# Optimization experiments

Measured on AMD Instinct MI355X. Metric: run time of the kernel, lower is better.

The kernel has to match this reference:

```python
import jax, jax.numpy as jnp
import numpy as np

B, F_IN, T_IN = 256, 3, 800
C, K, H, N_OUT = 128, 15, 150, 10

def hard_sigmoid(x):
    # Keras-style hard sigmoid used by LSTMHardSigmoid: clamp(0.2*x + 0.5, 0, 1)
    return jnp.clip(0.2 * x + 0.5, 0.0, 1.0)

def setup_inputs() -> dict:
    key = jax.random.key(0)
    ks = jax.random.split(key, 16)
    mk = lambda k, s, sc=0.05: (jax.random.normal(k, s, dtype=jnp.float32) * sc)
    return {
        "x": jax.random.normal(ks[0], (B, F_IN, T_IN), dtype=jnp.float32),
        "conv_w": mk(ks[1], (C, F_IN, K), 0.1),
        "conv_b": jnp.zeros((C,), jnp.float32),
        # PyTorch LSTM layout: [4H, in] with gate order i,f,g,o
        "w_ih_f": mk(ks[2], (4 * H, C)),
        "w_hh_f": mk(ks[3], (4 * H, H)),
        "b_ih_f": mk(ks[4], (4 * H,)),
        "b_hh_f": mk(ks[5], (4 * H,)),
        "w_ih_b": mk(ks[6], (4 * H, C)),
        "w_hh_b": mk(ks[7], (4 * H, H)),
        "b_ih_b": mk(ks[8], (4 * H,)),
        "b_hh_b": mk(ks[9], (4 * H,)),
        "lin1_w": mk(ks[10], (50, 2 * H)),
        "lin1_b": jnp.zeros((50,), jnp.float32),
        "lin2_w": mk(ks[11], (N_OUT, 50)),
        "lin2_b": jnp.zeros((N_OUT,), jnp.float32),
    }

def _lstm_dir(xseq, w_ih, w_hh, b_ih, b_hh, reverse):
    # xseq: [B, T, C] -> pre-activations [B, T, 4H]
    pre = jnp.einsum('btc,gc->btg', xseq, w_ih) + b_ih + b_hh
    pre_t = jnp.swapaxes(pre, 0, 1)  # [T, B, 4H]
    h0 = jnp.zeros((xseq.shape[0], H), pre.dtype)
    c0 = jnp.zeros((xseq.shape[0], H), pre.dtype)
    def step(carry, gt):
        h, c = carry
        g = gt + h @ w_hh.T
        i, f, gg, o = jnp.split(g, 4, axis=-1)
        c = hard_sigmoid(f) * c + hard_sigmoid(i) * jnp.tanh(gg)
        h = hard_sigmoid(o) * jnp.tanh(c)
        return (h, c), h
    _, hs = jax.lax.scan(step, (h0, c0), pre_t, reverse=reverse)
    return jnp.swapaxes(hs, 0, 1)  # [B, T, H]

def reference(x, conv_w, conv_b, w_ih_f, w_hh_f, b_ih_f, b_hh_f,
              w_ih_b, w_hh_b, b_ih_b, b_hh_b, lin1_w, lin1_b, lin2_w, lin2_b):
    # net1: Conv1d (VALID) + ReLU + (Dropout: identity at eval) + MaxPool1d(2)
    y = jax.lax.conv_general_dilated(
        x, conv_w, window_strides=(1,), padding='VALID',
        dimension_numbers=('NCH', 'OIH', 'NCH')) + conv_b[None, :, None]
    y = jax.nn.relu(y)                       # [B, 128, 786]
    L = y.shape[2] // 2
    y = y[:, :, :2 * L].reshape(y.shape[0], y.shape[1], L, 2).max(axis=-1)  # [B,128,393]
    xseq = jnp.transpose(y, (0, 2, 1))       # [B, 393, 128]
    # net2: bidirectional LSTM with hard-sigmoid gates
    h_fwd = _lstm_dir(xseq, w_ih_f, w_hh_f, b_ih_f, b_hh_f, reverse=False)
    h_bwd = _lstm_dir(xseq, w_ih_b, w_hh_b, b_ih_b, b_hh_b, reverse=True)
    bi = jnp.concatenate([h_fwd, h_bwd], axis=-1)  # [B, T, 300]
    # global max-pool over time (F.max_pool1d with kernel = full length)
    pooled = bi.max(axis=1)                  # [B, 300]
    # net3: Linear + ReLU + (Dropout identity) + Linear + Softmax(dim=1)
    z = jax.nn.relu(pooled @ lin1_w.T + lin1_b)
    logits = z @ lin2_w.T + lin2_b
    return jax.nn.softmax(logits, axis=1)
```

## Files before the change

kernel.cpp:

```cpp
#include <hip/hip_runtime.h>
#include <cstdio>

#define BATCH 256
#define TSEQ  393
#define CH    128
#define FIN   3
#define TIN   800
#define KK    15
#define HID   150
#define NPAD  640
#define KPAD  160
#define NB    16
#define PHASE 131
#define SLOTSTRIDE (256*640)

typedef _Float16 half_t;
typedef __attribute__((ext_vector_type(8))) _Float16 h8v;
typedef __attribute__((ext_vector_type(4))) _Float16 h4v;
typedef __attribute__((ext_vector_type(4))) float f4v;

__device__ inline float hsig(float x){
  return __builtin_amdgcn_fmed3f(fmaf(0.2f, x, 0.5f), 0.f, 1.f);
}
__device__ inline float tanh_(float x){
  float e = __expf(2.f*x);
  return fmaf(-2.f, __builtin_amdgcn_rcpf(e + 1.f), 1.f);
}

__global__ __launch_bounds__(256) void setup(const float* __restrict__ x,
    const float* __restrict__ conv_w, const float* __restrict__ conv_b,
    const float* __restrict__ wihf, const float* __restrict__ whhf,
    const float* __restrict__ bihf, const float* __restrict__ bhhf,
    const float* __restrict__ wihb, const float* __restrict__ whhb,
    const float* __restrict__ bihb, const float* __restrict__ bhhb,
    half_t* __restrict__ xseq, half_t* __restrict__ wih, half_t* __restrict__ whh,
    float* __restrict__ bsum){
  __shared__ float wl[CH*FIN*KK];
  __shared__ float xl[FIN][78];
  int bx = blockIdx.x, tid = threadIdx.x;
  if (bx < 3328){
    int b = bx & 255, t0 = (bx >> 8)*32;
    for (int i = tid; i < CH*FIN*KK; i += 256) wl[i] = conv_w[i];
    int p0 = 2*t0;
    for (int i = tid; i < FIN*78; i += 256){
      int f = i/78, q = i%78; int p = p0 + q;
      xl[f][q] = (p < TIN) ? x[((size_t)b*FIN + f)*TIN + p] : 0.f;
    }
    __syncthreads();
    int c = tid & 127, th = tid >> 7;
    float a0[16], a1[16];
    #pragma unroll
    for (int i=0;i<16;++i){ a0[i]=0.f; a1[i]=0.f; }
    #pragma unroll
    for (int f=0; f<FIN; ++f){
      float xv[46];
      #pragma unroll
      for (int q=0;q<46;++q) xv[q] = xl[f][th*32 + q];
      #pragma unroll
      for (int k=0;k<KK;++k){
        float ws = wl[c*FIN*KK + f*KK + k];
        #pragma unroll
        for (int i=0;i<16;++i){
          a0[i] = fmaf(xv[2*i+k],   ws, a0[i]);
          a1[i] = fmaf(xv[2*i+k+1], ws, a1[i]);
        }
      }
    }
    float bc = conv_b[c];
    #pragma unroll
    for (int i=0;i<16;++i){
      int t = t0 + th*16 + i;
      if (t < TSEQ){
        float v = fmaxf(fmaxf(a0[i], a1[i]) + bc, 0.f);
        xseq[((size_t)b*TSEQ + t)*CH + c] = (half_t)v;
      }
    }
    return;
  }
  bx -= 3328;
  if (bx < 640){
    int i = bx*256 + tid;
    int c = i & 127; int n = (i >> 7) % NPAD; int d = i / (NPAD*CH);
    const float* src = d ? wihb : wihf;
    float v = 0.f;
    if (n < 600){ int j = n >> 2, g = n & 3; v = src[(g*HID + j)*CH + c]; }
    wih[i] = (half_t)v;
    return;
  }
  bx -= 640;
  if (bx < 800){
    int i = bx*256 + tid;
    int kc = i % KPAD; int n = (i / KPAD) % NPAD; int d = i / (NPAD*KPAD);
    const float* src = d ? whhb : whhf;
    float v = 0.f;
    if (n < 600 && kc < HID){ int j = n >> 2, g = n & 3; v = src[(g*HID + j)*HID + kc]; }
    whh[i] = (half_t)v;
    return;
  }
  { int i = (bx-800)*256 + tid;
    if (i < 2*NPAD){
      int n = i % NPAD; int d = i / NPAD;
      float v = 0.f;
      if (n < 600){ int j = n >> 2, g = n & 3; int r = g*HID + j;
        v = d ? (bihb[r] + bhhb[r]) : (bihf[r] + bhhf[r]); }
      bsum[i] = v;
    }
  }
}

__device__ __forceinline__ void proj_body(const half_t* __restrict__ xseq,
    const half_t* __restrict__ wih, const float* __restrict__ bsum,
    half_t* __restrict__ pre, int off, int nproj, int idx){
  int bt4 = idx & 3; int rest = idx >> 2;
  int s = rest % nproj; int d = rest / nproj;
  int sg = s + off;
  int t = d ? (TSEQ-1 - sg) : sg;
  int tid = threadIdx.x, wv = tid >> 6, ln = tid & 63;
  int m = ln & 15, kg = ln >> 4;
  half_t* pslot = pre + ((size_t)d*PHASE + s)*SLOTSTRIDE;
  #pragma unroll
  for (int i = 0; i < 5; ++i){
    int nt = (wv*5 + i)*16;
    h8v bfr[4];
    #pragma unroll
    for (int ks = 0; ks < 4; ++ks)
      bfr[ks] = *(const h8v*)(wih + ((size_t)d*NPAD + nt + m)*CH + ks*32 + kg*8);
    f4v bs4 = *(const f4v*)(bsum + d*NPAD + nt + kg*4);
    #pragma unroll
    for (int ms = 0; ms < 4; ++ms){
      int b = bt4*64 + ms*16 + m;
      h8v ax[4];
      #pragma unroll
      for (int ks = 0; ks < 4; ++ks)
        ax[ks] = *(const h8v*)(xseq + ((size_t)b*TSEQ + t)*CH + ks*32 + kg*8);
      f4v acc = bs4;
      #pragma unroll
      for (int ks = 0; ks < 4; ++ks)
        acc = __builtin_amdgcn_mfma_f32_16x16x32_f16(bfr[ks], ax[ks], acc, 0, 0, 0);
      h4v hv = {(half_t)acc[0], (half_t)acc[1], (half_t)acc[2], (half_t)acc[3]};
      *(h4v*)(pslot + (size_t)b*640 + nt + kg*4) = hv;
    }
  }
}

__global__ __launch_bounds__(512) void proj_kernel(const half_t* __restrict__ xseq,
    const half_t* __restrict__ wih, const float* __restrict__ bsum,
    half_t* __restrict__ pre, int off, int nproj){
  proj_body(xseq, wih, bsum, pre, off, nproj, blockIdx.x);
}

#define PIN4(R0,R1,R2,R3, V) asm volatile( \
  "v_accvgpr_write_b32 " R0 ", %0\n\t" \
  "v_accvgpr_write_b32 " R1 ", %1\n\t" \
  "v_accvgpr_write_b32 " R2 ", %2\n\t" \
  "v_accvgpr_write_b32 " R3 ", %3" \
  :: "v"(V[0]), "v"(V[1]), "v"(V[2]), "v"(V[3]) : R0, R1, R2, R3)

#define LP(I,KS, R0,R1,R2,R3) { \
  h8v w_ = *(const h8v*)(whh + ((size_t)d*NPAD + ((wv*5+(I))*16+m))*KPAD + (KS)*32 + kg*8); \
  f4v wf_; __builtin_memcpy(&wf_, &w_, 16); \
  PIN4(R0,R1,R2,R3, wf_); }

#define ACLOBS "a0","a1","a2","a3","a4","a5","a6","a7","a8","a9",\
"a10","a11","a12","a13","a14","a15","a16","a17","a18","a19",\
"a20","a21","a22","a23","a24","a25","a26","a27","a28","a29",\
"a30","a31","a32","a33","a34","a35","a36","a37","a38","a39",\
"a40","a41","a42","a43","a44","a45","a46","a47","a48","a49",\
"a50","a51","a52","a53","a54","a55","a56","a57","a58","a59",\
"a60","a61","a62","a63","a64","a65","a66","a67","a68","a69",\
"a70","a71","a72","a73","a74","a75","a76","a77","a78","a79",\
"a80","a81","a82","a83","a84","a85","a86","a87","a88","a89",\
"a90","a91","a92","a93","a94","a95","a96","a97","a98","a99"

__global__ __launch_bounds__(512, 2) void recur_fused(
    const half_t* __restrict__ preR, const half_t* __restrict__ whh,
    float* __restrict__ pooled, float* __restrict__ stateC, half_t* __restrict__ stateH,
    int first, int last,
    const half_t* __restrict__ xseq, const half_t* __restrict__ wih,
    const float* __restrict__ bsum, half_t* __restrict__ preW,
    int off_next, int nproj){
  __shared__ __align__(16) half_t hbuf[2*NB*168];

  if (blockIdx.x >= 32){
    if (nproj > 0) proj_body(xseq, wih, bsum, preW, off_next, nproj, blockIdx.x - 32);
    return;
  }

  int tid = threadIdx.x, wv = tid >> 6, ln = tid & 63;
  int m = ln & 15, kg = ln >> 4;
  int bl = m;
  int bt = blockIdx.x & 15, d = blockIdx.x >> 4;
  int b0 = bt*NB;
  int blk = d*16 + bt;

  LP(0,0,"a0","a1","a2","a3")    LP(0,1,"a4","a5","a6","a7")    LP(0,2,"a8","a9","a10","a11")
  LP(0,3,"a12","a13","a14","a15") LP(0,4,"a16","a17","a18","a19")
  LP(1,0,"a20","a21","a22","a23") LP(1,1,"a24","a25","a26","a27") LP(1,2,"a28","a29","a30","a31")
  LP(1,3,"a32","a33","a34","a35") LP(1,4,"a36","a37","a38","a39")
  LP(2,0,"a40","a41","a42","a43") LP(2,1,"a44","a45","a46","a47") LP(2,2,"a48","a49","a50","a51")
  LP(2,3,"a52","a53","a54","a55") LP(2,4,"a56","a57","a58","a59")
  LP(3,0,"a60","a61","a62","a63") LP(3,1,"a64","a65","a66","a67") LP(3,2,"a68","a69","a70","a71")
  LP(3,3,"a72","a73","a74","a75") LP(3,4,"a76","a77","a78","a79")
  LP(4,0,"a80","a81","a82","a83") LP(4,1,"a84","a85","a86","a87") LP(4,2,"a88","a89","a90","a91")
  LP(4,3,"a92","a93","a94","a95") LP(4,4,"a96","a97","a98","a99")

  int jb = wv*20 + kg;

  float c_reg[5], hm_reg[5];
  if (first){
    for (int i = tid; i < 2*NB*168; i += 512) hbuf[i] = (half_t)0.f;
    #pragma unroll
    for (int T = 0; T < 5; ++T){ c_reg[T] = 0.f; hm_reg[T] = -1e30f; }
  } else {
    for (int i = tid; i < NB*168; i += 512) hbuf[i] = stateH[(size_t)blk*NB*168 + i];
    for (int i = tid; i < NB*168; i += 512) hbuf[NB*168 + i] = (half_t)0.f;
    const float* sc = stateC + ((size_t)blk*512 + tid)*10;
    #pragma unroll
    for (int T = 0; T < 5; ++T){ c_reg[T] = sc[T]; hm_reg[T] = sc[5+T]; }
  }
  __syncthreads();

  const half_t* pb = preR + (size_t)d*PHASE*SLOTSTRIDE + (size_t)b0*640;
  int pofl = bl*640 + wv*80 + kg*4;

  h4v curp[5], nA[5];
  #pragma unroll
  for (int T = 0; T < 5; ++T) curp[T] = *(const h4v*)(pb + pofl + T*16);
  {
    const half_t* p1 = pb + (size_t)SLOTSTRIDE;
    #pragma unroll
    for (int T = 0; T < 5; ++T) nA[T] = *(const h4v*)(p1 + pofl + T*16);
  }

  int p = 0;
  #pragma unroll 1
  for (int s = 0; s < PHASE; ++s){
    int s2 = (s+2 < PHASE) ? s+2 : PHASE-1;
    const half_t* p2 = pb + (size_t)s2*SLOTSTRIDE;
    h4v nB[5];
    #pragma unroll
    for (int T = 0; T < 5; ++T) nB[T] = *(const h4v*)(p2 + pofl + T*16);

    const half_t* hrd = hbuf + p*NB*168 + bl*168;
    h8v ah0 = *(const h8v*)(hrd + 0*32 + kg*8);
    h8v ah1 = *(const h8v*)(hrd + 1*32 + kg*8);
    h8v ah2 = *(const h8v*)(hrd + 2*32 + kg*8);
    h8v ah3 = *(const h8v*)(hrd + 3*32 + kg*8);
    h8v ah4 = *(const h8v*)(hrd + 4*32 + kg*8);

    f4v acc0 = {(float)curp[0][0], (float)curp[0][1], (float)curp[0][2], (float)curp[0][3]};
    f4v acc1 = {(float)curp[1][0], (float)curp[1][1], (float)curp[1][2], (float)curp[1][3]};
    f4v acc2 = {(float)curp[2][0], (float)curp[2][1], (float)curp[2][2], (float)curp[2][3]};
    f4v acc3 = {(float)curp[3][0], (float)curp[3][1], (float)curp[3][2], (float)curp[3][3]};
    f4v acc4 = {(float)curp[4][0], (float)curp[4][1], (float)curp[4][2], (float)curp[4][3]};

    asm volatile(
      "s_nop 1\n\t"
      "v_mfma_f32_16x16x32_f16 %0, a[0:3], %5, %0\n\t"
      "v_mfma_f32_16x16x32_f16 %1, a[20:23], %5, %1\n\t"
      "v_mfma_f32_16x16x32_f16 %2, a[40:43], %5, %2\n\t"
      "v_mfma_f32_16x16x32_f16 %3, a[60:63], %5, %3\n\t"
      "v_mfma_f32_16x16x32_f16 %4, a[80:83], %5, %4\n\t"
      "v_mfma_f32_16x16x32_f16 %0, a[4:7], %6, %0\n\t"
      "v_mfma_f32_16x16x32_f16 %1, a[24:27], %6, %1\n\t"
      "v_mfma_f32_16x16x32_f16 %2, a[44:47], %6, %2\n\t"
      "v_mfma_f32_16x16x32_f16 %3, a[64:67], %6, %3\n\t"
      "v_mfma_f32_16x16x32_f16 %4, a[84:87], %6, %4\n\t"
      "v_mfma_f32_16x16x32_f16 %0, a[8:11], %7, %0\n\t"
      "v_mfma_f32_16x16x32_f16 %1, a[28:31], %7, %1\n\t"
      "v_mfma_f32_16x16x32_f16 %2, a[48:51], %7, %2\n\t"
      "v_mfma_f32_16x16x32_f16 %3, a[68:71], %7, %3\n\t"
      "v_mfma_f32_16x16x32_f16 %4, a[88:91], %7, %4\n\t"
      "v_mfma_f32_16x16x32_f16 %0, a[12:15], %8, %0\n\t"
      "v_mfma_f32_16x16x32_f16 %1, a[32:35], %8, %1\n\t"
      "v_mfma_f32_16x16x32_f16 %2, a[52:55], %8, %2\n\t"
      "v_mfma_f32_16x16x32_f16 %3, a[72:75], %8, %3\n\t"
      "v_mfma_f32_16x16x32_f16 %4, a[92:95], %8, %4\n\t"
      "v_mfma_f32_16x16x32_f16 %0, a[16:19], %9, %0\n\t"
      "v_mfma_f32_16x16x32_f16 %1, a[36:39], %9, %1\n\t"
      "v_mfma_f32_16x16x32_f16 %2, a[56:59], %9, %2\n\t"
      "v_mfma_f32_16x16x32_f16 %3, a[76:79], %9, %3\n\t"
      "v_mfma_f32_16x16x32_f16 %4, a[96:99], %9, %4\n\t"
      "s_nop 7\n\t"
      "s_nop 7"
      : "+v"(acc0), "+v"(acc1), "+v"(acc2), "+v"(acc3), "+v"(acc4)
      : "v"(ah0), "v"(ah1), "v"(ah2), "v"(ah3), "v"(ah4));
    __builtin_amdgcn_sched_barrier(0);

    half_t* hwr = hbuf + (p^1)*NB*168 + bl*168 + jb;
    #define GATE(A, T) { \
      float cn = hsig(A[1])*c_reg[T] + hsig(A[0])*tanh_(A[2]); \
      float hn = hsig(A[3])*tanh_(cn); \
      c_reg[T] = cn; hm_reg[T] = fmaxf(hm_reg[T], hn); \
      hwr[(T)*4] = (half_t)hn; }
    GATE(acc0, 0) GATE(acc1, 1) GATE(acc2, 2) GATE(acc3, 3) GATE(acc4, 4)
    #undef GATE

    #pragma unroll
    for (int T = 0; T < 5; ++T) curp[T] = nA[T];
    #pragma unroll
    for (int T = 0; T < 5; ++T) nA[T] = nB[T];

    asm volatile("s_waitcnt lgkmcnt(0)" ::: "memory", ACLOBS);
    __builtin_amdgcn_s_barrier();
    __builtin_amdgcn_sched_barrier(0);
    p ^= 1;
  }

  if (!last){
    for (int i = tid; i < NB*168; i += 512) stateH[(size_t)blk*NB*168 + i] = hbuf[p*NB*168 + i];
    float* sc = stateC + ((size_t)blk*512 + tid)*10;
    #pragma unroll
    for (int T = 0; T < 5; ++T){ sc[T] = c_reg[T]; sc[5+T] = hm_reg[T]; }
  } else {
    #pragma unroll
    for (int T = 0; T < 5; ++T){
      int j = jb + T*4;
      if (j < HID) pooled[(size_t)(b0 + bl)*300 + d*HID + j] = hm_reg[T];
    }
  }
}

__global__ __launch_bounds__(256) void fc(const float* __restrict__ pooled,
                                          const float* __restrict__ w1, const float* __restrict__ b1,
                                          const float* __restrict__ w2, const float* __restrict__ b2,
                                          float* __restrict__ out){
  __shared__ float prow[300];
  __shared__ float ps[64][5];
  __shared__ float z[52];
  __shared__ float lg[12];
  int b = blockIdx.x, tid = threadIdx.x;
  for (int i = tid; i < 300; i += 256) prow[i] = pooled[(size_t)b*300 + i];
  __syncthreads();
  int j = tid & 63, seg = tid >> 6;
  float a = 0.f;
  if (j < 50){
    const float* wr = w1 + (size_t)j*300 + seg*75;
    const float* pr = prow + seg*75;
    #pragma unroll 5
    for (int k = 0; k < 75; ++k) a = fmaf(pr[k], wr[k], a);
  }
  ps[j][seg] = a;
  __syncthreads();
  if (tid < 50) z[tid] = fmaxf(ps[tid][0]+ps[tid][1]+ps[tid][2]+ps[tid][3] + b1[tid], 0.f);
  __syncthreads();
  if (tid < 10){
    float a2 = b2[tid];
    for (int k = 0; k < 50; ++k) a2 = fmaf(z[k], w2[tid*50 + k], a2);
    lg[tid] = a2;
  }
  __syncthreads();
  if (tid < 10){
    float mx = lg[0];
    #pragma unroll
    for (int k = 1; k < 10; ++k) mx = fmaxf(mx, lg[k]);
    float ssum = 0.f;
    #pragma unroll
    for (int k = 0; k < 10; ++k) ssum += __expf(lg[k] - mx);
    out[(size_t)b*10 + tid] = __expf(lg[tid] - mx) / ssum;
  }
}

extern "C" void kernel_launch(void* const* d_in, const int* in_sizes, int n_in,
                              void* d_out, int out_size, void* d_ws, size_t ws_size,
                              hipStream_t stream) {
  const float* x      = (const float*)d_in[0];
  const float* conv_w = (const float*)d_in[1];
  const float* conv_b = (const float*)d_in[2];
  const float* w_ih_f = (const float*)d_in[3];
  const float* w_hh_f = (const float*)d_in[4];
  const float* b_ih_f = (const float*)d_in[5];
  const float* b_hh_f = (const float*)d_in[6];
  const float* w_ih_b = (const float*)d_in[7];
  const float* w_hh_b = (const float*)d_in[8];
  const float* b_ih_b = (const float*)d_in[9];
  const float* b_hh_b = (const float*)d_in[10];
  const float* l1w = (const float*)d_in[11];
  const float* l1b = (const float*)d_in[12];
  const float* l2w = (const float*)d_in[13];
  const float* l2b = (const float*)d_in[14];
  float* out = (float*)d_out;

  char* ws = (char*)d_ws;
  size_t off = 0;
  auto alloc = [&](size_t bytes){ size_t o = off; off += (bytes + 255) & ~(size_t)255; return o; };
  size_t xseq_o = alloc((size_t)BATCH*TSEQ*CH*2);
  size_t preA_o = alloc((size_t)2*PHASE*SLOTSTRIDE*2);
  size_t preB_o = alloc((size_t)2*PHASE*SLOTSTRIDE*2);
  size_t wih_o  = alloc((size_t)2*NPAD*CH*2);
  size_t whh_o  = alloc((size_t)2*NPAD*KPAD*2);
  size_t bs_o   = alloc((size_t)2*NPAD*4);
  size_t pool_o = alloc((size_t)BATCH*300*4);
  size_t stc_o  = alloc((size_t)32*512*10*4);
  size_t sth_o  = alloc((size_t)32*NB*168*2);
  if (off > ws_size){
    fprintf(stderr, "[cnnblstm] WS TOO SMALL: need %zu have %zu\n", off, ws_size);
    return;
  }
  half_t* xseq_p = (half_t*)(ws + xseq_o);
  half_t* preA_p = (half_t*)(ws + preA_o);
  half_t* preB_p = (half_t*)(ws + preB_o);
  half_t* wih_p  = (half_t*)(ws + wih_o);
  half_t* whh_p  = (half_t*)(ws + whh_o);
  float*  bs_p   = (float*)(ws + bs_o);
  float*  pool_p = (float*)(ws + pool_o);
  float*  stc_p  = (float*)(ws + stc_o);
  half_t* sth_p  = (half_t*)(ws + sth_o);

  int projBlocks = 4*PHASE*2;

  setup<<<3328 + 640 + 800 + 5, 256, 0, stream>>>(x, conv_w, conv_b,
      w_ih_f, w_hh_f, b_ih_f, b_hh_f, w_ih_b, w_hh_b, b_ih_b, b_hh_b,
      xseq_p, wih_p, whh_p, bs_p);
  proj_kernel<<<projBlocks, 512, 0, stream>>>(xseq_p, wih_p, bs_p, preA_p, 0, PHASE);
  recur_fused<<<32 + projBlocks, 512, 0, stream>>>(preA_p, whh_p, pool_p, stc_p, sth_p,
      1, 0, xseq_p, wih_p, bs_p, preB_p, PHASE, PHASE);
  recur_fused<<<32 + projBlocks, 512, 0, stream>>>(preB_p, whh_p, pool_p, stc_p, sth_p,
      0, 0, xseq_p, wih_p, bs_p, preA_p, 2*PHASE, PHASE);
  recur_fused<<<32, 512, 0, stream>>>(preA_p, whh_p, pool_p, stc_p, sth_p,
      0, 1, xseq_p, wih_p, bs_p, preB_p, 0, 0);

  fc<<<BATCH, 256, 0, stream>>>(pool_p, l1w, l1b, l2w, l2b, out);
}
```

Measured before the change: 599.9 us.

## Stage recurrent pre-activations through LDS with async global-to-LDS loads and swizzle

The recurrent kernel now brings each step's pre-activation slice into a triple-buffered LDS stage using global_load_lds DMA, two steps ahead. Before, each thread loaded it into registers itself. The projection writer XOR-swizzles columns by batch row so the LDS reads avoid bank conflicts, and the h buffer row stride is padded from 168 to 170. The aim is to take global-load latency and VGPR pressure off the serial recurrence critical path. In exchange the kernel uses much more LDS (about 60KB), which may limit co-residency with the fused projection blocks, and correctness depends on per-wave vmcnt accounting.

```diff
diff --git a/kernel.cpp b/kernel.cpp
--- a/kernel.cpp
+++ b/kernel.cpp
@@ -13,6 +13,7 @@
 #define NB    16
 #define PHASE 131
 #define SLOTSTRIDE (256*640)
+#define HSTR  170
 
 typedef _Float16 half_t;
 typedef __attribute__((ext_vector_type(8))) _Float16 h8v;
@@ -25,6 +26,12 @@
 __device__ inline float tanh_(float x){
   float e = __expf(2.f*x);
   return fmaf(-2.f, __builtin_amdgcn_rcpf(e + 1.f), 1.f);
+}
+
+__device__ __forceinline__ void gload_lds16(const half_t* g, half_t* l){
+  __builtin_amdgcn_global_load_lds(
+      (const __attribute__((address_space(1))) void*)g,
+      (__attribute__((address_space(3))) void*)l, 16, 0, 0);
 }
 
 __global__ __launch_bounds__(256) void setup(const float* __restrict__ x,
@@ -138,7 +145,8 @@
       for (int ks = 0; ks < 4; ++ks)
         acc = __builtin_amdgcn_mfma_f32_16x16x32_f16(bfr[ks], ax[ks], acc, 0, 0, 0);
       h4v hv = {(half_t)acc[0], (half_t)acc[1], (half_t)acc[2], (half_t)acc[3]};
-      *(h4v*)(pslot + (size_t)b*640 + nt + kg*4) = hv;
+      int q = (nt + kg*4) ^ ((b & 7) << 3);
+      *(h4v*)(pslot + (size_t)b*640 + q) = hv;
     }
   }
 }
@@ -179,7 +187,8 @@
     const half_t* __restrict__ xseq, const half_t* __restrict__ wih,
     const float* __restrict__ bsum, half_t* __restrict__ preW,
     int off_next, int nproj){
-  __shared__ __align__(16) half_t hbuf[2*NB*168];
+  __shared__ __align__(16) half_t hbuf[2*NB*HSTR];
+  __shared__ __align__(16) half_t stage[3*NB*640];
 
   if (blockIdx.x >= 32){
     if (nproj > 0) proj_body(xseq, wih, bsum, preW, off_next, nproj, blockIdx.x - 32);
@@ -208,51 +217,61 @@
 
   float c_reg[5], hm_reg[5];
   if (first){
-    for (int i = tid; i < 2*NB*168; i += 512) hbuf[i] = (half_t)0.f;
+    for (int i = tid; i < 2*NB*HSTR; i += 512) hbuf[i] = (half_t)0.f;
     #pragma unroll
     for (int T = 0; T < 5; ++T){ c_reg[T] = 0.f; hm_reg[T] = -1e30f; }
   } else {
-    for (int i = tid; i < NB*168; i += 512) hbuf[i] = stateH[(size_t)blk*NB*168 + i];
-    for (int i = tid; i < NB*168; i += 512) hbuf[NB*168 + i] = (half_t)0.f;
+    for (int i = tid; i < NB*HSTR; i += 512) hbuf[i] = stateH[(size_t)blk*NB*HSTR + i];
+    for (int i = tid; i < NB*HSTR; i += 512) hbuf[NB*HSTR + i] = (half_t)0.f;
     const float* sc = stateC + ((size_t)blk*512 + tid)*10;
     #pragma unroll
     for (int T = 0; T < 5; ++T){ c_reg[T] = sc[T]; hm_reg[T] = sc[5+T]; }
   }
-  __syncthreads();
 
   const half_t* pb = preR + (size_t)d*PHASE*SLOTSTRIDE + (size_t)b0*640;
-  int pofl = bl*640 + wv*80 + kg*4;
-
-  h4v curp[5], nA[5];
-  #pragma unroll
-  for (int T = 0; T < 5; ++T) curp[T] = *(const h4v*)(pb + pofl + T*16);
-  {
-    const half_t* p1 = pb + (size_t)SLOTSTRIDE;
-    #pragma unroll
-    for (int T = 0; T < 5; ++T) nA[T] = *(const h4v*)(p1 + pofl + T*16);
-  }
+  int swz = (bl & 7) << 3;
+
+  #define ISSUE(GS, SL) do{ \
+    const half_t* g_ = (GS); half_t* l_ = stage + (SL)*(NB*640); \
+    if (wv < 4){ \
+      _Pragma("unroll") for (int q_ = 0; q_ < 3; ++q_){ int k_ = wv*3 + q_; \
+        gload_lds16(g_ + k_*512 + ln*8, l_ + k_*512); } \
+    } else { \
+      _Pragma("unroll") for (int q_ = 0; q_ < 2; ++q_){ int k_ = 12 + (wv-4)*2 + q_; \
+        gload_lds16(g_ + k_*512 + ln*8, l_ + k_*512); } \
+    } }while(0)
+
+  ISSUE(pb, 0);
+  ISSUE(pb + SLOTSTRIDE, 1);
+  if (wv < 4) asm volatile("s_waitcnt vmcnt(3) lgkmcnt(0)" ::: "memory");
+  else        asm volatile("s_waitcnt vmcnt(2) lgkmcnt(0)" ::: "memory");
+  __builtin_amdgcn_s_barrier();
+  __builtin_amdgcn_sched_barrier(0);
 
   int p = 0;
   #pragma unroll 1
   for (int s = 0; s < PHASE; ++s){
-    int s2 = (s+2 < PHASE) ? s+2 : PHASE-1;
-    const half_t* p2 = pb + (size_t)s2*SLOTSTRIDE;
-    h4v nB[5];
-    #pragma unroll
-    for (int T = 0; T < 5; ++T) nB[T] = *(const h4v*)(p2 + pofl + T*16);
-
-    const half_t* hrd = hbuf + p*NB*168 + bl*168;
+    if (s + 2 < PHASE) ISSUE(pb + (size_t)(s+2)*SLOTSTRIDE, (s+2)%3);
+
+    const half_t* srow = stage + (s%3)*(NB*640) + bl*640;
+    h4v p40 = *(const h4v*)(srow + (((wv*5+0)*16 + kg*4) ^ swz));
+    h4v p41 = *(const h4v*)(srow + (((wv*5+1)*16 + kg*4) ^ swz));
+    h4v p42 = *(const h4v*)(srow + (((wv*5+2)*16 + kg*4) ^ swz));
+    h4v p43 = *(const h4v*)(srow + (((wv*5+3)*16 + kg*4) ^ swz));
+    h4v p44 = *(const h4v*)(srow + (((wv*5+4)*16 + kg*4) ^ swz));
+
+    const half_t* hrd = hbuf + p*NB*HSTR + bl*HSTR;
     h8v ah0 = *(const h8v*)(hrd + 0*32 + kg*8);
     h8v ah1 = *(const h8v*)(hrd + 1*32 + kg*8);
     h8v ah2 = *(const h8v*)(hrd + 2*32 + kg*8);
     h8v ah3 = *(const h8v*)(hrd + 3*32 + kg*8);
     h8v ah4 = *(const h8v*)(hrd + 4*32 + kg*8);
 
-    f4v acc0 = {(float)curp[0][0], (float)curp[0][1], (float)curp[0][2], (float)curp[0][3]};
-    f4v acc1 = {(float)curp[1][0], (float)curp[1][1], (float)curp[1][2], (float)curp[1][3]};
-    f4v acc2 = {(float)curp[2][0], (float)curp[2][1], (float)curp[2][2], (float)curp[2][3]};
-    f4v acc3 = {(float)curp[3][0], (float)curp[3][1], (float)curp[3][2], (float)curp[3][3]};
-    f4v acc4 = {(float)curp[4][0], (float)curp[4][1], (float)curp[4][2], (float)curp[4][3]};
+    f4v acc0 = {(float)p40[0], (float)p40[1], (float)p40[2], (float)p40[3]};
+    f4v acc1 = {(float)p41[0], (float)p41[1], (float)p41[2], (float)p41[3]};
+    f4v acc2 = {(float)p42[0], (float)p42[1], (float)p42[2], (float)p42[3]};
+    f4v acc3 = {(float)p43[0], (float)p43[1], (float)p43[2], (float)p43[3]};
+    f4v acc4 = {(float)p44[0], (float)p44[1], (float)p44[2], (float)p44[3]};
 
     asm volatile(
       "s_nop 1\n\t"
@@ -287,7 +306,7 @@
       : "v"(ah0), "v"(ah1), "v"(ah2), "v"(ah3), "v"(ah4));
     __builtin_amdgcn_sched_barrier(0);
 
-    half_t* hwr = hbuf + (p^1)*NB*168 + bl*168 + jb;
+    half_t* hwr = hbuf + (p^1)*NB*HSTR + bl*HSTR + jb;
     #define GATE(A, T) { \
       float cn = hsig(A[1])*c_reg[T] + hsig(A[0])*tanh_(A[2]); \
       float hn = hsig(A[3])*tanh_(cn); \
@@ -296,19 +315,16 @@
     GATE(acc0, 0) GATE(acc1, 1) GATE(acc2, 2) GATE(acc3, 3) GATE(acc4, 4)
     #undef GATE
 
-    #pragma unroll
-    for (int T = 0; T < 5; ++T) curp[T] = nA[T];
-    #pragma unroll
-    for (int T = 0; T < 5; ++T) nA[T] = nB[T];
-
-    asm volatile("s_waitcnt lgkmcnt(0)" ::: "memory", ACLOBS);
+    if (wv < 4) asm volatile("s_waitcnt vmcnt(3) lgkmcnt(0)" ::: "memory", ACLOBS);
+    else        asm volatile("s_waitcnt vmcnt(2) lgkmcnt(0)" ::: "memory", ACLOBS);
     __builtin_amdgcn_s_barrier();
     __builtin_amdgcn_sched_barrier(0);
     p ^= 1;
   }
+  #undef ISSUE
 
   if (!last){
-    for (int i = tid; i < NB*168; i += 512) stateH[(size_t)blk*NB*168 + i] = hbuf[p*NB*168 + i];
+    for (int i = tid; i < NB*HSTR; i += 512) stateH[(size_t)blk*NB*HSTR + i] = hbuf[p*NB*HSTR + i];
     float* sc = stateC + ((size_t)blk*512 + tid)*10;
     #pragma unroll
     for (int T = 0; T < 5; ++T){ sc[T] = c_reg[T]; sc[5+T] = hm_reg[T]; }
@@ -392,7 +408,7 @@
   size_t bs_o   = alloc((size_t)2*NPAD*4);
   size_t pool_o = alloc((size_t)BATCH*300*4);
   size_t stc_o  = alloc((size_t)32*512*10*4);
-  size_t sth_o  = alloc((size_t)32*NB*168*2);
+  size_t sth_o  = alloc((size_t)32*NB*HSTR*2);
   if (off > ws_size){
     fprintf(stderr, "[cnnblstm] WS TOO SMALL: need %zu have %zu\n", off, ws_size);
     return;
```

After: 1.015 ms. 69.2% more time.
